# Kernel tuning notes

Measured on AMD Instinct MI355X. Metric: run time of the kernel, lower is better.

The kernel has to match this reference:

```python
import jax, jax.numpy as jnp
import numpy as np

NEG = -10000000000.0  # matches the torch module's additive mask value


def _span_attn(enc, logit_tok, starts, ends, qb, bsz):
    # enc: [bsz, seq, d]; logit_tok: [bsz, seq]; starts/ends/qb: [Q]
    seq = enc.shape[1]
    pos = jnp.arange(seq)
    # span mask: token t belongs to span iff start <= t <= end (inclusive)
    mask = (pos[None, :] >= starts[:, None]) & (pos[None, :] <= ends[:, None])  # [Q, seq]
    logits = logit_tok[qb] + (1.0 - mask.astype(enc.dtype)) * NEG               # [Q, seq]
    w = jax.nn.softmax(logits, axis=1)                                           # [Q, seq]
    # avoid materializing enc[qb] ([Q, seq, d]): contract against every batch row,
    # then select the right batch with a one-hot (p is tiny: [Q, bsz, d]).
    p = jnp.einsum('qs,bsd->qbd', w, enc)
    oh = jax.nn.one_hot(qb, bsz, dtype=enc.dtype)
    return jnp.einsum('qbd,qb->qd', p, oh)


def setup_inputs() -> dict:
    key = jax.random.key(0)
    ks = jax.random.split(key, 10)
    bsz, seq, hd, pd, Q = 8, 2048, 1024, 256, 8192
    enc = jax.random.normal(ks[0], (bsz, seq, hd), dtype=jnp.float32)
    proj_w = jax.random.normal(ks[1], (hd, pd), dtype=jnp.float32) * (1.0 / np.sqrt(hd))
    proj_b = jnp.zeros((pd,), dtype=jnp.float32)
    attn_w = jax.random.normal(ks[2], (pd,), dtype=jnp.float32) * (1.0 / np.sqrt(pd))
    attn_b = jnp.zeros((), dtype=jnp.float32)

    def make_spans(k):
        k1, k2, k3 = jax.random.split(k, 3)
        s = jax.random.randint(k1, (Q,), 0, seq)
        ln = jax.random.randint(k2, (Q,), 0, 32)
        e = jnp.minimum(s + ln, seq - 1)
        return s, e

    s1, e1 = make_spans(ks[3])
    s2, e2 = make_spans(ks[4])
    qb = jax.random.randint(ks[5], (Q,), 0, bsz)
    return {
        'flag': 0,
        'encoded_input': enc,
        'start_ids_1': s1,
        'end_ids_1': e1,
        'query_batch_idx': qb,
        'start_ids_2': s2,
        'end_ids_2': e2,
        'proj_w': proj_w,
        'proj_b': proj_b,
        'attn_w': attn_w,
        'attn_b': attn_b,
    }


def reference(flag, encoded_input, start_ids_1, end_ids_1, query_batch_idx,
              start_ids_2, end_ids_2, proj_w, proj_b, attn_w, attn_b):
    del flag  # unused in the original forward
    bsz = encoded_input.shape[0]
    enc = encoded_input @ proj_w + proj_b                 # use_proj=True path
    logit_tok = jnp.einsum('bsd,d->bs', enc, attn_w) + attn_b  # Linear(d,1)
    res1 = _span_attn(enc, logit_tok, start_ids_1, end_ids_1, query_batch_idx, bsz)
    res2 = _span_attn(enc, logit_tok, start_ids_2, end_ids_2, query_batch_idx, bsz)
    return (res1, res2)
```

## Files before the change

### kernel.cpp

```cpp
#include <hip/hip_runtime.h>

typedef __attribute__((ext_vector_type(8))) short bf16x8;
typedef __attribute__((ext_vector_type(4))) float f32x4;

#define LDK 40

__device__ __forceinline__ float bf2f(unsigned short u) {
    union { unsigned int i; float f; } v; v.i = ((unsigned int)u) << 16; return v.f;
}
__device__ __forceinline__ unsigned short f2bf(float f) {
    union { float f; unsigned int i; } v; v.f = f;
    unsigned int x = v.i;
    return (unsigned short)((x + 0x7FFFu + ((x >> 16) & 1u)) >> 16);
}

__device__ __forceinline__ void gload16(const void* g, void* l) {
    __builtin_amdgcn_global_load_lds(
        (const __attribute__((address_space(1))) unsigned int*)g,
        (__attribute__((address_space(3))) unsigned int*)l, 16, 0, 0);
}

#define ASM_LGKM0 { asm volatile("s_waitcnt lgkmcnt(0)" ::: "memory"); \
                    __builtin_amdgcn_sched_barrier(0); }
#define ASM_BAR   asm volatile("s_barrier" ::: "memory")

__global__ __launch_bounds__(256) void transpose_b_kernel(
    const float* __restrict__ B, unsigned short* __restrict__ Bt, int K, int N)
{
    __shared__ float tile[32][33];
    int kb = blockIdx.x % (K / 32);
    int nb = blockIdx.x / (K / 32);
    int k0 = kb * 32, n0 = nb * 32;
    int tx = threadIdx.x & 31, ty = threadIdx.x >> 5;
    #pragma unroll
    for (int i = 0; i < 4; ++i)
        tile[ty + 8 * i][tx] = B[(size_t)(k0 + ty + 8 * i) * N + n0 + tx];
    __syncthreads();
    #pragma unroll
    for (int i = 0; i < 4; ++i)
        Bt[(size_t)(n0 + ty + 8 * i) * K + k0 + tx] = f2bf(tile[tx][ty + 8 * i]);
}

__global__ __launch_bounds__(256, 4) void gemm_mfma_kernel(
    const float* __restrict__ A, const unsigned short* __restrict__ Bt,
    const float* __restrict__ bias, const float* __restrict__ attn_w,
    unsigned short* __restrict__ C, float* __restrict__ logit,
    int M, int N, int K)
{
    __shared__ __attribute__((aligned(16))) unsigned short AsA[2][64 * LDK];
    __shared__ __attribute__((aligned(16))) unsigned short AsB[2][64 * 32];

    const int tid = threadIdx.x;
    const int bid = blockIdx.x;
    const int xcd = bid & 7;
    const int j   = bid >> 3;
    const int bn  = (j & 3) * 64;
    const int bm  = (xcd * 32 + (j >> 2)) * 64;

    const int lane = tid & 63;
    const int wave = tid >> 6;
    const int wr = (wave >> 1) * 32;
    const int wc = (wave & 1) * 32;

    const int srow = tid >> 2;
    const int sk   = (tid & 3) * 8;
    const float* Aptr = A + (size_t)(bm + srow) * K + sk;

    const int brow = 16 * wave + (lane >> 2);
    const int bsl  = (lane & 3) ^ ((lane >> 3) & 3);
    const unsigned short* Bptr = Bt + (size_t)(bn + brow) * K + bsl * 8;
    unsigned short* ldsB0 = &AsB[0][wave * 512];
    unsigned short* ldsB1 = &AsB[1][wave * 512];

    float4 areg[2][2];
    f32x4 acc[2][2];
    #pragma unroll
    for (int m = 0; m < 2; ++m)
        #pragma unroll
        for (int n = 0; n < 2; ++n)
            acc[m][n] = (f32x4){0.f, 0.f, 0.f, 0.f};

    const int c15 = lane & 15;
    const int g4  = lane >> 4;
    const int kg8 = g4 * 8;
    const int slB = (g4 ^ ((c15 >> 1) & 3)) * 8;

    const int nk = K / 32;

    gload16(Bptr, ldsB0);
    areg[0][0] = *(const float4*)(Aptr);
    areg[0][1] = *(const float4*)(Aptr + 4);
    asm volatile("s_waitcnt vmcnt(0)" ::: "memory");
    {
        unsigned short tmp[8];
        const float* afp = (const float*)areg[0];
        #pragma unroll
        for (int i = 0; i < 8; ++i) tmp[i] = f2bf(afp[i]);
        *(bf16x8*)&AsA[0][srow * LDK + sk] = *(bf16x8*)&tmp[0];
    }
    gload16(Bptr + 32, ldsB1);
    areg[1][0] = *(const float4*)(Aptr + 32);
    areg[1][1] = *(const float4*)(Aptr + 36);
    ASM_LGKM0;
    ASM_BAR;

#define BODY(T, S)                                                            \
    {                                                                         \
        bf16x8 af0 = *(bf16x8*)&AsA[S][(wr + c15) * LDK + kg8];               \
        bf16x8 af1 = *(bf16x8*)&AsA[S][(wr + 16 + c15) * LDK + kg8];          \
        bf16x8 bf0 = *(bf16x8*)&AsB[S][(wc + c15) * 32 + slB];                \
        bf16x8 bf1 = *(bf16x8*)&AsB[S][(wc + 16 + c15) * 32 + slB];           \
        ASM_LGKM0;                                                            \
        ASM_BAR;                            \
        if ((T) + 2 < nk) {                                                   \
            gload16(Bptr + ((T) + 2) * 32, (S) ? ldsB1 : ldsB0);              \
            areg[S][0] = *(const float4*)(Aptr + ((T) + 2) * 32);             \
            areg[S][1] = *(const float4*)(Aptr + ((T) + 2) * 32 + 4);         \
        }                                                                     \
        __builtin_amdgcn_s_setprio(1);                                        \
        acc[0][0] = __builtin_amdgcn_mfma_f32_16x16x32_bf16(af0, bf0, acc[0][0], 0, 0, 0); \
        acc[0][1] = __builtin_amdgcn_mfma_f32_16x16x32_bf16(af0, bf1, acc[0][1], 0, 0, 0); \
        acc[1][0] = __builtin_amdgcn_mfma_f32_16x16x32_bf16(af1, bf0, acc[1][0], 0, 0, 0); \
        acc[1][1] = __builtin_amdgcn_mfma_f32_16x16x32_bf16(af1, bf1, acc[1][1], 0, 0, 0); \
        __builtin_amdgcn_s_setprio(0);                                        \
        if ((T) + 1 < nk) {                                                   \
            if ((T) + 2 < nk) { asm volatile("s_waitcnt vmcnt(3)" ::: "memory"); } \
            else              { asm volatile("s_waitcnt vmcnt(0)" ::: "memory"); } \
            unsigned short tmp[8];                                            \
            const float* afp = (const float*)areg[1 - (S)];                   \
            _Pragma("unroll")                                                 \
            for (int i = 0; i < 8; ++i) tmp[i] = f2bf(afp[i]);                \
            *(bf16x8*)&AsA[1 - (S)][srow * LDK + sk] = *(bf16x8*)&tmp[0];     \
            ASM_LGKM0;                                                        \
        }                                                                     \
        ASM_BAR;                                           \
    }

    for (int t = 0; t < nk; t += 2) {
        BODY(t, 0)
        BODY(t + 1, 1)
    }
#undef BODY

    const int col0 = bn + wc + c15;
    const int row0 = bm + wr + g4 * 4;
    float wsum[2][4] = {};
    #pragma unroll
    for (int n = 0; n < 2; ++n) {
        float bv  = bias[col0 + n * 16];
        float awv = attn_w[col0 + n * 16];
        #pragma unroll
        for (int m = 0; m < 2; ++m) {
            #pragma unroll
            for (int i = 0; i < 4; ++i) {
                float cf = acc[m][n][i] + bv;
                C[(size_t)(row0 + m * 16 + i) * N + col0 + n * 16] = f2bf(cf);
                wsum[m][i] += cf * awv;
            }
        }
    }
    #pragma unroll
    for (int m = 0; m < 2; ++m) {
        #pragma unroll
        for (int i = 0; i < 4; ++i) {
            float v = wsum[m][i];
            v += __shfl_xor(v, 1, 64);
            v += __shfl_xor(v, 2, 64);
            v += __shfl_xor(v, 4, 64);
            v += __shfl_xor(v, 8, 64);
            if (c15 == 0) atomicAdd(&logit[row0 + m * 16 + i], v);
        }
    }
}

__global__ __launch_bounds__(256) void span_kernel(
    const unsigned short* __restrict__ enc, const float* __restrict__ logit,
    const int* __restrict__ s1, const int* __restrict__ e1,
    const int* __restrict__ s2, const int* __restrict__ e2,
    const int* __restrict__ qb, float* __restrict__ out,
    int Q, int seq, int pd)
{
    int lane = threadIdx.x & 63;
    int q = blockIdx.x * 4 + (threadIdx.x >> 6);
    int r  = (q >= Q) ? 1 : 0;
    int qi = q - r * Q;
    int s = r ? s2[qi] : s1[qi];
    int e = r ? e2[qi] : e1[qi];
    int b = qb[qi];
    int len = e - s + 1;

    const float* lp = logit + (size_t)b * seq + s;
    float lg = (lane < len) ? lp[lane] : -3.4e38f;
    float m = lg;
    #pragma unroll
    for (int off = 32; off; off >>= 1) m = fmaxf(m, __shfl_xor(m, off, 64));
    float p = (lane < len) ? __expf(lg - m) : 0.0f;
    float sum = p;
    #pragma unroll
    for (int off = 32; off; off >>= 1) sum += __shfl_xor(sum, off, 64);
    float inv = 1.0f / sum;

    const unsigned short* ep = enc + ((size_t)b * seq + s) * pd + lane * 4;
    float ax = 0.f, ay = 0.f, az = 0.f, aw = 0.f;

    for (int t0 = 0; t0 < len; t0 += 16) {
        ushort4 ev[16];
        #pragma unroll
        for (int u = 0; u < 16; ++u) {
            int tc = t0 + u;
            tc = (tc < len) ? tc : (len - 1);
            ev[u] = *(const ushort4*)(ep + (size_t)tc * pd);
        }
        #pragma unroll
        for (int u = 0; u < 16; ++u) {
            float wt = __shfl(p, t0 + u, 64);
            ax += wt * bf2f(ev[u].x);
            ay += wt * bf2f(ev[u].y);
            az += wt * bf2f(ev[u].z);
            aw += wt * bf2f(ev[u].w);
        }
    }
    float4 res = {ax * inv, ay * inv, az * inv, aw * inv};
    *((float4*)(out + (size_t)q * pd) + lane) = res;
}

extern "C" void kernel_launch(void* const* d_in, const int* in_sizes, int n_in,
                              void* d_out, int out_size, void* d_ws, size_t ws_size,
                              hipStream_t stream) {
    const float* enc_in = (const float*)d_in[1];
    const int*   s1     = (const int*)d_in[2];
    const int*   e1     = (const int*)d_in[3];
    const int*   qb     = (const int*)d_in[4];
    const int*   s2     = (const int*)d_in[5];
    const int*   e2     = (const int*)d_in[6];
    const float* proj_w = (const float*)d_in[7];
    const float* proj_b = (const float*)d_in[8];
    const float* attn_w = (const float*)d_in[9];
    float* out = (float*)d_out;

    const int Q   = in_sizes[2];
    const int pd  = in_sizes[8];
    const int hd  = in_sizes[7] / pd;
    const int seq = 2048;
    const int M   = in_sizes[1] / hd;

    unsigned short* enc_bf = (unsigned short*)d_ws;
    float*          logit  = (float*)((char*)d_ws + (size_t)M * pd * 2);
    unsigned short* Btw    = (unsigned short*)((char*)d_ws +
                               (size_t)M * pd * 2 + (size_t)M * 4);

    hipMemsetAsync(logit, 0, (size_t)M * sizeof(float), stream);
    transpose_b_kernel<<<(hd / 32) * (pd / 32), 256, 0, stream>>>(proj_w, Btw, hd, pd);
    gemm_mfma_kernel<<<(M / 64) * (pd / 64), 256, 0, stream>>>(
        enc_in, Btw, proj_b, attn_w, enc_bf, logit, M, pd, hd);
    span_kernel<<<2 * Q / 4, 256, 0, stream>>>(
        enc_bf, logit, s1, e1, s2, e2, qb, out, Q, seq, pd);
}
```

Baseline: 172.7 us.

## Restructure projection GEMM: 64x128 tiles, direct-register A loads, triple-buffered B

The projection GEMM tile grows from 64x64 to 64x128 with a K step of 64, and each wave now computes a 32x64 sub-tile (2x4 MFMA fragments). The A operand (fp32 activations) is loaded straight into registers in fragment layout and converted to bf16 in place, so it no longer takes a round trip through LDS. B tiles are triple-buffered in LDS with an XOR swizzle, loads are issued two steps ahead, and there is one barrier per K step. The goal is less LDS traffic and fewer barriers per FLOP plus more loads in flight, at the cost of higher register pressure (launch bounds cut from 4 to 2 blocks per CU) and half as many blocks.

Measured after the change: 177.1 us. +2.6%, slower.

```diff
diff --git a/kernel.cpp b/kernel.cpp
--- a/kernel.cpp
+++ b/kernel.cpp
@@ -2,8 +2,6 @@
 
 typedef __attribute__((ext_vector_type(8))) short bf16x8;
 typedef __attribute__((ext_vector_type(4))) float f32x4;
-
-#define LDK 40
 
 __device__ __forceinline__ float bf2f(unsigned short u) {
     union { unsigned int i; float f; } v; v.i = ((unsigned int)u) << 16; return v.f;
@@ -13,7 +11,6 @@
     unsigned int x = v.i;
     return (unsigned short)((x + 0x7FFFu + ((x >> 16) & 1u)) >> 16);
 }
-
 __device__ __forceinline__ void gload16(const void* g, void* l) {
     __builtin_amdgcn_global_load_lds(
         (const __attribute__((address_space(1))) unsigned int*)g,
@@ -22,6 +19,7 @@
 
 #define ASM_LGKM0 { asm volatile("s_waitcnt lgkmcnt(0)" ::: "memory"); \
                     __builtin_amdgcn_sched_barrier(0); }
+#define ASM_VM(N) asm volatile("s_waitcnt vmcnt(" #N ")" ::: "memory")
 #define ASM_BAR   asm volatile("s_barrier" ::: "memory")
 
 __global__ __launch_bounds__(256) void transpose_b_kernel(
@@ -41,134 +39,165 @@
         Bt[(size_t)(n0 + ty + 8 * i) * K + k0 + tx] = f2bf(tile[tx][ty + 8 * i]);
 }
 
-__global__ __launch_bounds__(256, 4) void gemm_mfma_kernel(
+__global__ __launch_bounds__(256, 2) void gemm_mfma_kernel(
     const float* __restrict__ A, const unsigned short* __restrict__ Bt,
     const float* __restrict__ bias, const float* __restrict__ attn_w,
     unsigned short* __restrict__ C, float* __restrict__ logit,
     int M, int N, int K)
 {
-    __shared__ __attribute__((aligned(16))) unsigned short AsA[2][64 * LDK];
-    __shared__ __attribute__((aligned(16))) unsigned short AsB[2][64 * 32];
+    __shared__ __attribute__((aligned(16))) char BufB[3 * 16384];
 
     const int tid = threadIdx.x;
     const int bid = blockIdx.x;
     const int xcd = bid & 7;
     const int j   = bid >> 3;
-    const int bn  = (j & 3) * 64;
-    const int bm  = (xcd * 32 + (j >> 2)) * 64;
+    const int bn  = (j & 1) * 128;
+    const int bm  = (xcd * 32 + (j >> 1)) * 64;
 
     const int lane = tid & 63;
     const int wave = tid >> 6;
-    const int wr = (wave >> 1) * 32;
-    const int wc = (wave & 1) * 32;
-
-    const int srow = tid >> 2;
-    const int sk   = (tid & 3) * 8;
-    const float* Aptr = A + (size_t)(bm + srow) * K + sk;
-
-    const int brow = 16 * wave + (lane >> 2);
-    const int bsl  = (lane & 3) ^ ((lane >> 3) & 3);
-    const unsigned short* Bptr = Bt + (size_t)(bn + brow) * K + bsl * 8;
-    unsigned short* ldsB0 = &AsB[0][wave * 512];
-    unsigned short* ldsB1 = &AsB[1][wave * 512];
-
-    float4 areg[2][2];
-    f32x4 acc[2][2];
-    #pragma unroll
-    for (int m = 0; m < 2; ++m)
-        #pragma unroll
-        for (int n = 0; n < 2; ++n)
-            acc[m][n] = (f32x4){0.f, 0.f, 0.f, 0.f};
-
+    const int wr = (wave & 1) * 32;
+    const int wc = (wave >> 1) * 64;
     const int c15 = lane & 15;
     const int g4  = lane >> 4;
-    const int kg8 = g4 * 8;
-    const int slB = (g4 ^ ((c15 >> 1) & 3)) * 8;
-
-    const int nk = K / 32;
-
-    gload16(Bptr, ldsB0);
-    areg[0][0] = *(const float4*)(Aptr);
-    areg[0][1] = *(const float4*)(Aptr + 4);
-    asm volatile("s_waitcnt vmcnt(0)" ::: "memory");
-    {
-        unsigned short tmp[8];
-        const float* afp = (const float*)areg[0];
-        #pragma unroll
-        for (int i = 0; i < 8; ++i) tmp[i] = f2bf(afp[i]);
-        *(bf16x8*)&AsA[0][srow * LDK + sk] = *(bf16x8*)&tmp[0];
-    }
-    gload16(Bptr + 32, ldsB1);
-    areg[1][0] = *(const float4*)(Aptr + 32);
-    areg[1][1] = *(const float4*)(Aptr + 36);
-    ASM_LGKM0;
+
+    const float* Ar0 = A + (size_t)(bm + wr + c15) * K + g4 * 8;
+    const float* Ar1 = A + (size_t)(bm + wr + 16 + c15) * K + g4 * 8;
+
+    const int bn_l   = wave * 32 + (lane >> 3);
+    const int bslot  = (lane & 7) ^ ((lane >> 3) & 7);
+    const unsigned short* Bsrc = Bt + (size_t)(bn + bn_l) * K + bslot * 8;
+    char* ldsW = BufB + wave * 4096;
+
+    int offB[4][2];
+    #pragma unroll
+    for (int nf = 0; nf < 4; ++nf)
+        #pragma unroll
+        for (int ks = 0; ks < 2; ++ks)
+            offB[nf][ks] = (wc + nf * 16 + c15) * 128 + (((ks * 4 + g4) ^ (c15 & 7)) * 16);
+
+    f32x4 acc[2][4];
+    #pragma unroll
+    for (int mf = 0; mf < 2; ++mf)
+        #pragma unroll
+        for (int nf = 0; nf < 4; ++nf)
+            acc[mf][nf] = (f32x4){0.f, 0.f, 0.f, 0.f};
+
+    float4 aq0[8], aq1[8];
+    const int nk = K / 64;
+
+#define ISSUE_A(T, AQ)                                                        \
+    {                                                                         \
+        const float* a0 = Ar0 + (T) * 64;                                     \
+        const float* a1 = Ar1 + (T) * 64;                                     \
+        AQ[0] = *(const float4*)(a0);       AQ[1] = *(const float4*)(a0 + 4); \
+        AQ[2] = *(const float4*)(a0 + 32);  AQ[3] = *(const float4*)(a0 + 36);\
+        AQ[4] = *(const float4*)(a1);       AQ[5] = *(const float4*)(a1 + 4); \
+        AQ[6] = *(const float4*)(a1 + 32);  AQ[7] = *(const float4*)(a1 + 36);\
+    }
+#define ISSUE_B(T, BOFF)                                                      \
+    {                                                                         \
+        const unsigned short* s = Bsrc + (T) * 64;                            \
+        char* d = ldsW + (BOFF);                                              \
+        gload16(s,             d);                                            \
+        gload16(s +  8 * K,    d + 1024);                                     \
+        gload16(s + 16 * K,    d + 2048);                                     \
+        gload16(s + 24 * K,    d + 3072);                                     \
+    }
+#define CVT_MFMA(AQ, BROFF)                                                   \
+    {                                                                         \
+        bf16x8 bfr[4][2];                                                     \
+        _Pragma("unroll")                                                     \
+        for (int nf = 0; nf < 4; ++nf)                                        \
+            _Pragma("unroll")                                                 \
+            for (int ks = 0; ks < 2; ++ks)                                    \
+                bfr[nf][ks] = *(bf16x8*)(BufB + (BROFF) + offB[nf][ks]);      \
+        bf16x8 afr[2][2];                                                     \
+        _Pragma("unroll")                                                     \
+        for (int mf = 0; mf < 2; ++mf)                                        \
+            _Pragma("unroll")                                                 \
+            for (int ks = 0; ks < 2; ++ks) {                                  \
+                unsigned short tmp[8];                                        \
+                const float* f0 = (const float*)&AQ[mf * 4 + ks * 2];         \
+                _Pragma("unroll")                                             \
+                for (int i = 0; i < 8; ++i) tmp[i] = f2bf(f0[i]);             \
+                afr[mf][ks] = *(bf16x8*)&tmp[0];                              \
+            }                                                                 \
+        ASM_LGKM0;                                                            \
+        __builtin_amdgcn_s_setprio(1);                                        \
+        _Pragma("unroll")                                                     \
+        for (int ks = 0; ks < 2; ++ks)                                        \
+            _Pragma("unroll")                                                 \
+            for (int mf = 0; mf < 2; ++mf)                                    \
+                _Pragma("unroll")                                             \
+                for (int nf = 0; nf < 4; ++nf)                                \
+                    acc[mf][nf] = __builtin_amdgcn_mfma_f32_16x16x32_bf16(    \
+                        afr[mf][ks], bfr[nf][ks], acc[mf][nf], 0, 0, 0);      \
+        __builtin_amdgcn_s_setprio(0);                                        \
+    }
+
+    ISSUE_A(0, aq0) ISSUE_B(0, 0)
+    ISSUE_A(1, aq1) ISSUE_B(1, 16384)
+
+    int br = 0, bw = 32768;
+
+#define BODY(T, AQ)                                                           \
+    {                                                                         \
+        ASM_VM(12);        \
+        ASM_BAR;                        \
+        if ((T) + 2 < nk) {                                                   \
+            ISSUE_B((T) + 2, bw)                                              \
+        }                                                                     \
+        CVT_MFMA(AQ, br)                                                      \
+        if ((T) + 2 < nk) {                                                   \
+            ISSUE_A((T) + 2, AQ)                                              \
+        }                                                                     \
+        br += 16384; if (br == 49152) br = 0;                                 \
+        bw += 16384; if (bw == 49152) bw = 0;                                 \
+    }
+
+    int t = 0;
+    for (; t + 2 < nk; t += 2) {
+        BODY(t, aq0)
+        BODY(t + 1, aq1)
+    }
+    BODY(t, aq0)
+    ASM_VM(0);
     ASM_BAR;
-
-#define BODY(T, S)                                                            \
-    {                                                                         \
-        bf16x8 af0 = *(bf16x8*)&AsA[S][(wr + c15) * LDK + kg8];               \
-        bf16x8 af1 = *(bf16x8*)&AsA[S][(wr + 16 + c15) * LDK + kg8];          \
-        bf16x8 bf0 = *(bf16x8*)&AsB[S][(wc + c15) * 32 + slB];                \
-        bf16x8 bf1 = *(bf16x8*)&AsB[S][(wc + 16 + c15) * 32 + slB];           \
-        ASM_LGKM0;                                                            \
-        ASM_BAR;                            \
-        if ((T) + 2 < nk) {                                                   \
-            gload16(Bptr + ((T) + 2) * 32, (S) ? ldsB1 : ldsB0);              \
-            areg[S][0] = *(const float4*)(Aptr + ((T) + 2) * 32);             \
-            areg[S][1] = *(const float4*)(Aptr + ((T) + 2) * 32 + 4);         \
-        }                                                                     \
-        __builtin_amdgcn_s_setprio(1);                                        \
-        acc[0][0] = __builtin_amdgcn_mfma_f32_16x16x32_bf16(af0, bf0, acc[0][0], 0, 0, 0); \
-        acc[0][1] = __builtin_amdgcn_mfma_f32_16x16x32_bf16(af0, bf1, acc[0][1], 0, 0, 0); \
-        acc[1][0] = __builtin_amdgcn_mfma_f32_16x16x32_bf16(af1, bf0, acc[1][0], 0, 0, 0); \
-        acc[1][1] = __builtin_amdgcn_mfma_f32_16x16x32_bf16(af1, bf1, acc[1][1], 0, 0, 0); \
-        __builtin_amdgcn_s_setprio(0);                                        \
-        if ((T) + 1 < nk) {                                                   \
-            if ((T) + 2 < nk) { asm volatile("s_waitcnt vmcnt(3)" ::: "memory"); } \
-            else              { asm volatile("s_waitcnt vmcnt(0)" ::: "memory"); } \
-            unsigned short tmp[8];                                            \
-            const float* afp = (const float*)areg[1 - (S)];                   \
-            _Pragma("unroll")                                                 \
-            for (int i = 0; i < 8; ++i) tmp[i] = f2bf(afp[i]);                \
-            *(bf16x8*)&AsA[1 - (S)][srow * LDK + sk] = *(bf16x8*)&tmp[0];     \
-            ASM_LGKM0;                                                        \
-        }                                                                     \
-        ASM_BAR;                                           \
-    }
-
-    for (int t = 0; t < nk; t += 2) {
-        BODY(t, 0)
-        BODY(t + 1, 1)
-    }
+    CVT_MFMA(aq1, br)
+
 #undef BODY
-
-    const int col0 = bn + wc + c15;
+#undef ISSUE_A
+#undef ISSUE_B
+#undef CVT_MFMA
+
     const int row0 = bm + wr + g4 * 4;
+    const int colb = bn + wc + c15;
     float wsum[2][4] = {};
     #pragma unroll
-    for (int n = 0; n < 2; ++n) {
-        float bv  = bias[col0 + n * 16];
-        float awv = attn_w[col0 + n * 16];
-        #pragma unroll
-        for (int m = 0; m < 2; ++m) {
+    for (int nf = 0; nf < 4; ++nf) {
+        float bv  = bias[colb + nf * 16];
+        float awv = attn_w[colb + nf * 16];
+        #pragma unroll
+        for (int mf = 0; mf < 2; ++mf) {
             #pragma unroll
             for (int i = 0; i < 4; ++i) {
-                float cf = acc[m][n][i] + bv;
-                C[(size_t)(row0 + m * 16 + i) * N + col0 + n * 16] = f2bf(cf);
-                wsum[m][i] += cf * awv;
+                float cf = acc[mf][nf][i] + bv;
+                C[(size_t)(row0 + mf * 16 + i) * N + colb + nf * 16] = f2bf(cf);
+                wsum[mf][i] += cf * awv;
             }
         }
     }
     #pragma unroll
-    for (int m = 0; m < 2; ++m) {
+    for (int mf = 0; mf < 2; ++mf) {
         #pragma unroll
         for (int i = 0; i < 4; ++i) {
-            float v = wsum[m][i];
+            float v = wsum[mf][i];
             v += __shfl_xor(v, 1, 64);
             v += __shfl_xor(v, 2, 64);
             v += __shfl_xor(v, 4, 64);
             v += __shfl_xor(v, 8, 64);
-            if (c15 == 0) atomicAdd(&logit[row0 + m * 16 + i], v);
+            if (c15 == 0) atomicAdd(&logit[row0 + mf * 16 + i], v);
         }
     }
 }
@@ -244,14 +273,14 @@
     const int seq = 2048;
     const int M   = in_sizes[1] / hd;
 
-    unsigned short* enc_bf = (unsigned short*)d_ws;
-    float*          logit  = (float*)((char*)d_ws + (size_t)M * pd * 2);
-    unsigned short* Btw    = (unsigned short*)((char*)d_ws +
-                               (size_t)M * pd * 2 + (size_t)M * 4);
+    char* ws = (char*)d_ws;
+    unsigned short* enc_bf = (unsigned short*)ws;   ws += (size_t)M * pd * 2;
+    float*          logit  = (float*)ws;            ws += (size_t)M * 4;
+    unsigned short* Btw    = (unsigned short*)ws;   ws += (size_t)pd * hd * 2;
 
     hipMemsetAsync(logit, 0, (size_t)M * sizeof(float), stream);
     transpose_b_kernel<<<(hd / 32) * (pd / 32), 256, 0, stream>>>(proj_w, Btw, hd, pd);
-    gemm_mfma_kernel<<<(M / 64) * (pd / 64), 256, 0, stream>>>(
+    gemm_mfma_kernel<<<(M / 64) * (pd / 128), 256, 0, stream>>>(
         enc_in, Btw, proj_b, attn_w, enc_bf, logit, M, pd, hd);
     span_kernel<<<2 * Q / 4, 256, 0, stream>>>(
         enc_bf, logit, s1, e1, s2, e2, qb, out, Q, seq, pd);
```
